# Optimization experiments

Measured on AMD Instinct MI355X. Metric: run time of the kernel, lower is better.

Reference implementation:

```python
import jax, jax.numpy as jnp
import numpy as np

N, D, K, V, H, F_ = 4096, 128, 64, 64, 4, 256
EPS = 1e-5


def _layer_norm(x, g, b):
    m = jnp.mean(x, axis=-1, keepdims=True)
    v = jnp.mean((x - m) ** 2, axis=-1, keepdims=True)
    return (x - m) * jax.lax.rsqrt(v + EPS) * g + b


def setup_inputs() -> dict:
    key = jax.random.key(0)
    ks = jax.random.split(key, 20)
    s_in = (2.0 / D) ** 0.5  # kaiming-ish scale for q/k/v projections
    inp = {
        "x": jax.random.normal(ks[0], (N, D), jnp.float32),
        "rpe": jax.random.normal(ks[1], (5, N, N), jnp.float32) * 0.02,
        "Wq": jax.random.normal(ks[2], (H, D, K), jnp.float32) * s_in,
        "bq": jnp.zeros((H, K), jnp.float32),
        "Wk": jax.random.normal(ks[3], (H, D, K), jnp.float32) * s_in,
        "bk": jnp.zeros((H, K), jnp.float32),
        "Wv": jax.random.normal(ks[4], (H, D, V), jnp.float32) * s_in,
        "bv": jnp.zeros((H, V), jnp.float32),
        "rpe_w": jax.random.normal(ks[5], (5,), jnp.float32) * (1.0 / 5.0) ** 0.5,
        "rpe_b": jnp.zeros((), jnp.float32),
        "Wo": jax.random.normal(ks[6], (H * V, D), jnp.float32) * (1.0 / (H * V)) ** 0.5,
        "bo": jnp.zeros((D,), jnp.float32),
        "W1": jax.random.normal(ks[7], (D, F_), jnp.float32) * (1.0 / D) ** 0.5,
        "b1": jnp.zeros((F_,), jnp.float32),
        "W2": jax.random.normal(ks[8], (F_, D), jnp.float32) * (1.0 / F_) ** 0.5,
        "b2": jnp.zeros((D,), jnp.float32),
        "ln1_g": jnp.ones((D,), jnp.float32),
        "ln1_b": jnp.zeros((D,), jnp.float32),
        "ln2_g": jnp.ones((D,), jnp.float32),
        "ln2_b": jnp.zeros((D,), jnp.float32),
    }
    return inp


def reference(x, rpe, Wq, bq, Wk, bk, Wv, bv, rpe_w, rpe_b, Wo, bo,
              W1, b1, W2, b2, ln1_g, ln1_b, ln2_g, ln2_b):
    # ReLU'd per-head projections (vectorized over heads): [H, N, K/V]
    q = jax.nn.relu(jnp.einsum("nd,hdk->hnk", x, Wq) + bq[:, None, :])
    k = jax.nn.relu(jnp.einsum("nd,hdk->hnk", x, Wk) + bk[:, None, :])
    v = jax.nn.relu(jnp.einsum("nd,hdv->hnv", x, Wv) + bv[:, None, :])
    scores = jnp.einsum("hnk,hmk->hnm", q, k) / jnp.sqrt(jnp.asarray(K, x.dtype))
    attn = jax.nn.softmax(scores, axis=-1)  # torch dim=1 on 2D == last axis
    o = jnp.einsum("hnm,hmv->hnv", attn, v)
    mho = jnp.transpose(o, (1, 0, 2)).reshape(N, H * V)  # concat heads
    # RPE: Linear(5->1) over channel axis -> [N, N], then left-matmul
    rpe_weights = jnp.einsum("fnm,f->nm", rpe, rpe_w) + rpe_b
    adjusted = rpe_weights @ mho
    proj = adjusted @ Wo + bo
    x1 = _layer_norm(x + proj, ln1_g, ln1_b)  # dropout is identity (eval)
    ffn = jax.nn.relu(x1 @ W1 + b1) @ W2 + b2
    return _layer_norm(x1 + ffn, ln2_g, ln2_b)
```

## Files before the change

kernel.cpp:

```cpp
#include <hip/hip_runtime.h>

typedef __attribute__((ext_vector_type(8))) short bf16x8;
typedef __attribute__((ext_vector_type(4))) float f32x4;

#define N_TOK 4096
#define NC_ATT 8
#define NC_GEMM 8

static __device__ __forceinline__ ushort f2bf(float f) {
    union { float f; unsigned u; } x; x.f = f;
    unsigned u = x.u;
    unsigned r = (u + 0x7FFFu + ((u >> 16) & 1u)) >> 16;
    return (ushort)r;
}
static __device__ __forceinline__ unsigned pkbf(float a, float b) {
    unsigned r;
    asm("v_cvt_pk_bf16_f32 %0, %1, %2" : "=v"(r) : "v"(a), "v"(b));
    return r;
}
static __device__ __forceinline__ float bf2f(ushort u) {
    union { unsigned u; float f; } x; x.u = (unsigned)u << 16; return x.f;
}

__global__ void prep_all(const float* __restrict__ x,
                         const float* __restrict__ Wq, const float* __restrict__ Wk,
                         const float* __restrict__ Wv, const float* __restrict__ Wo,
                         const float* __restrict__ W1, const float* __restrict__ W2,
                         ushort* __restrict__ xb, ushort* __restrict__ WqT,
                         ushort* __restrict__ WkT, ushort* __restrict__ WvT,
                         ushort* __restrict__ WoT, ushort* __restrict__ W1T,
                         ushort* __restrict__ W2T) {
    int i = blockIdx.x * 256 + threadIdx.x;
    if (i < 131072) {
        float4 v = ((const float4*)x)[i];
        ushort4 o;
        o.x = f2bf(v.x); o.y = f2bf(v.y); o.z = f2bf(v.z); o.w = f2bf(v.w);
        ((ushort4*)xb)[i] = o;
        return;
    }
    int j = i - 131072;
    int t = j >> 15, e = j & 32767;
    if (t < 3) {
        const float* src = (t == 0 ? Wq : t == 1 ? Wk : Wv);
        ushort* dst = (t == 0 ? WqT : t == 1 ? WkT : WvT);
        int h = e >> 13, rem = e & 8191, d = rem >> 6, k = rem & 63;
        dst[h * 8192 + k * 128 + d] = f2bf(src[e]);
    } else if (t == 3) {
        int r = e >> 7, c = e & 127;
        WoT[c * 256 + r] = f2bf(Wo[e]);
    } else if (t == 4) {
        int r = e >> 8, c = e & 255;
        W1T[c * 128 + r] = f2bf(W1[e]);
    } else {
        int r = e >> 7, c = e & 127;
        W2T[c * 256 + r] = f2bf(W2[e]);
    }
}

__global__ __launch_bounds__(256) void qkv_proj(
    const ushort* __restrict__ xb, const ushort* __restrict__ WqT,
    const ushort* __restrict__ WkT, const ushort* __restrict__ WvT,
    const float* __restrict__ bq, const float* __restrict__ bk, const float* __restrict__ bv,
    ushort* __restrict__ qb, ushort* __restrict__ kb, ushort* __restrict__ vT) {
    int m0 = blockIdx.x * 64;
    int h = blockIdx.y & 3, which = blockIdx.y >> 2;
    int wave = threadIdx.x >> 6, lane = threadIdx.x & 63;
    int fr = lane & 15, kg = lane >> 4;
    int wm = m0 + wave * 16;
    const ushort* WT = (which == 0 ? WqT : which == 1 ? WkT : WvT) + (long)h * 64 * 128;
    const float* bias = (which == 0 ? bq : which == 1 ? bk : bv) + h * 64;
    f32x4 acc[4] = {};
    for (int k0 = 0; k0 < 128; k0 += 32) {
        bf16x8 a = *(const bf16x8*)(xb + (long)(wm + fr) * 128 + k0 + kg * 8);
#pragma unroll
        for (int t = 0; t < 4; ++t) {
            bf16x8 b = *(const bf16x8*)(WT + (long)(t * 16 + fr) * 128 + k0 + kg * 8);
            acc[t] = __builtin_amdgcn_mfma_f32_16x16x32_bf16(a, b, acc[t], 0, 0, 0);
        }
    }
    int rb = wm + kg * 4;
#pragma unroll
    for (int t = 0; t < 4; ++t) {
        int col = t * 16 + fr;
        float bs = bias[col];
        if (which == 2) {
            ushort4 o;
            o.x = f2bf(fmaxf(acc[t][0] + bs, 0.f));
            o.y = f2bf(fmaxf(acc[t][1] + bs, 0.f));
            o.z = f2bf(fmaxf(acc[t][2] + bs, 0.f));
            o.w = f2bf(fmaxf(acc[t][3] + bs, 0.f));
            *(ushort4*)(vT + ((long)h * 64 + col) * N_TOK + rb) = o;
        } else {
            ushort* dst = (which == 0 ? qb : kb) + (long)h * N_TOK * 64;
            float scl = (which == 0) ? 0.125f * 1.44269504f : 1.0f;
#pragma unroll
            for (int r = 0; r < 4; ++r)
                dst[(long)(rb + r) * 64 + col] = f2bf(fmaxf(acc[t][r] + bs, 0.f) * scl);
        }
    }
}

__global__ __launch_bounds__(512, 6) void attn_flash2(
    const ushort* __restrict__ qb, const ushort* __restrict__ kb,
    const ushort* __restrict__ vT, ushort* __restrict__ opart,
    float* __restrict__ mlpart) {
    int qt = blockIdx.x, h = blockIdx.y, cz = blockIdx.z;
    int w = threadIdx.x >> 6, lane = threadIdx.x & 63;
    int fr = lane & 15, kg = lane >> 4;
    int lr = lane >> 3, lc = lane & 7;
    int swz = (lc ^ (lr & 7)) * 8;
    __shared__ ushort Kt[2][64 * 64];
    __shared__ ushort Vt[2][64 * 64];
    __shared__ ushort Pl[8][16 * 64];
    const ushort* qh = qb + (long)h * N_TOK * 64;
    const ushort* kh = kb + (long)h * N_TOK * 64;
    const ushort* vh = vT + (long)h * 64 * N_TOK;
    int q0 = qt * 128 + w * 16;
    bf16x8 qf0 = *(const bf16x8*)(qh + (long)(q0 + fr) * 64 + kg * 8);
    bf16x8 qf1 = *(const bf16x8*)(qh + (long)(q0 + fr) * 64 + 32 + kg * 8);
    f32x4 o[4] = {};
    float lsum = 0.f;
    int nbase = cz * (N_TOK / NC_ATT);
    auto stage = [&](int buf, int s) {
        int n0 = nbase + s * 64;
        int row = w * 8 + lr;
        __builtin_amdgcn_global_load_lds(
            (const __attribute__((address_space(1))) unsigned int*)(kh + (long)(n0 + row) * 64 + swz),
            (__attribute__((address_space(3))) unsigned int*)(&Kt[buf][w * 512]), 16, 0, 0);
        __builtin_amdgcn_global_load_lds(
            (const __attribute__((address_space(1))) unsigned int*)(vh + (long)row * N_TOK + n0 + swz),
            (__attribute__((address_space(3))) unsigned int*)(&Vt[buf][w * 512]), 16, 0, 0);
    };
    stage(0, 0);
    __syncthreads();
    const int NS = (N_TOK / NC_ATT) / 64;
    for (int s = 0; s < NS; ++s) {
        int buf = s & 1;
        if (s + 1 < NS) stage(buf ^ 1, s + 1);
        f32x4 sc[4] = {};
        __builtin_amdgcn_s_setprio(1);
#pragma unroll
        for (int t = 0; t < 4; ++t) {
            int row = t * 16 + fr;
            bf16x8 k0 = *(const bf16x8*)(&Kt[buf][row * 64 + ((kg * 8) ^ ((row & 7) * 8))]);
            bf16x8 k1 = *(const bf16x8*)(&Kt[buf][row * 64 + ((32 + kg * 8) ^ ((row & 7) * 8))]);
            sc[t] = __builtin_amdgcn_mfma_f32_16x16x32_bf16(k0, qf0, sc[t], 0, 0, 0);
            sc[t] = __builtin_amdgcn_mfma_f32_16x16x32_bf16(k1, qf1, sc[t], 0, 0, 0);
        }
        __builtin_amdgcn_s_setprio(0);
#pragma unroll
        for (int t = 0; t < 4; ++t)
#pragma unroll
            for (int r = 0; r < 4; ++r) {
                float p = exp2f(sc[t][r]);
                sc[t][r] = p;
                lsum += p;
            }
#pragma unroll
        for (int t = 0; t < 4; ++t) {
            uint2 u;
            u.x = pkbf(sc[t][0], sc[t][1]);
            u.y = pkbf(sc[t][2], sc[t][3]);
            *(uint2*)(&Pl[w][fr * 64 + ((t * 16 + kg * 4) ^ ((fr & 7) * 8))]) = u;
        }
        __builtin_amdgcn_s_setprio(1);
#pragma unroll
        for (int ks = 0; ks < 2; ++ks) {
            bf16x8 pf = *(const bf16x8*)(&Pl[w][fr * 64 + ((ks * 32 + kg * 8) ^ ((fr & 7) * 8))]);
#pragma unroll
            for (int t = 0; t < 4; ++t) {
                int row = t * 16 + fr;
                bf16x8 b = *(const bf16x8*)(&Vt[buf][row * 64 + ((ks * 32 + kg * 8) ^ ((row & 7) * 8))]);
                o[t] = __builtin_amdgcn_mfma_f32_16x16x32_bf16(pf, b, o[t], 0, 0, 0);
            }
        }
        __builtin_amdgcn_s_setprio(0);
        __syncthreads();
    }
    lsum += __shfl_xor(lsum, 16);
    lsum += __shfl_xor(lsum, 32);
    float linv = 1.0f / lsum;
    float lq[4];
#pragma unroll
    for (int r = 0; r < 4; ++r) lq[r] = __shfl(linv, kg * 4 + r);
    ushort* ob = opart + (((long)cz * 4 + h) * N_TOK + q0 + kg * 4) * 64;
#pragma unroll
    for (int t = 0; t < 4; ++t)
#pragma unroll
        for (int r = 0; r < 4; ++r)
            ob[(long)r * 64 + t * 16 + fr] = f2bf(o[t][r] * lq[r]);
    if (lane < 16)
        mlpart[((long)cz * 4 + h) * N_TOK + q0 + lane] = lsum;
}

__global__ __launch_bounds__(256) void combine_wo(
    const ushort* __restrict__ opart, const float* __restrict__ mlpart,
    const ushort* __restrict__ WoT, ushort* __restrict__ PT) {
    int q0 = blockIdx.x * 16;
    int tid = threadIdx.x;
    __shared__ ushort mt[16 * 256];
    {
        int q = tid >> 4, cg = tid & 15;
        int h = cg >> 2;
        long qg = q0 + q;
        float L = 0.f, co[NC_ATT];
#pragma unroll
        for (int c = 0; c < NC_ATT; ++c) {
            co[c] = mlpart[((long)c * 4 + h) * N_TOK + qg];
            L += co[c];
        }
        float inv = 1.0f / L;
#pragma unroll
        for (int c = 0; c < NC_ATT; ++c) co[c] *= inv;
        float a[16];
#pragma unroll
        for (int j = 0; j < 16; ++j) a[j] = 0.f;
#pragma unroll
        for (int c = 0; c < NC_ATT; ++c) {
            const ushort* pr = opart + (((long)c * 4 + h) * N_TOK + qg) * 64 + (cg & 3) * 16;
            bf16x8 v0 = *(const bf16x8*)(pr);
            bf16x8 v1 = *(const bf16x8*)(pr + 8);
#pragma unroll
            for (int j = 0; j < 8; ++j) {
                a[j] += co[c] * bf2f((ushort)v0[j]);
                a[8 + j] += co[c] * bf2f((ushort)v1[j]);
            }
        }
        int c0 = cg * 16;
#pragma unroll
        for (int g = 0; g < 4; ++g) {
            uint2 u;
            u.x = pkbf(a[g * 4 + 0], a[g * 4 + 1]);
            u.y = pkbf(a[g * 4 + 2], a[g * 4 + 3]);
            *(uint2*)(&mt[q * 256 + ((c0 + g * 4) ^ ((q & 7) * 8))]) = u;
        }
    }
    __syncthreads();
    {
        int w = tid >> 6, lane = tid & 63;
        int fr = lane & 15, kg = lane >> 4;
        f32x4 acc[2] = {};
        for (int k0 = 0; k0 < 256; k0 += 32) {
            bf16x8 a0 = *(const bf16x8*)(WoT + (long)(w * 32 + fr) * 256 + k0 + kg * 8);
            bf16x8 a1 = *(const bf16x8*)(WoT + (long)(w * 32 + 16 + fr) * 256 + k0 + kg * 8);
            bf16x8 b = *(const bf16x8*)(&mt[fr * 256 + ((k0 + kg * 8) ^ ((fr & 7) * 8))]);
            acc[0] = __builtin_amdgcn_mfma_f32_16x16x32_bf16(a0, b, acc[0], 0, 0, 0);
            acc[1] = __builtin_amdgcn_mfma_f32_16x16x32_bf16(a1, b, acc[1], 0, 0, 0);
        }
#pragma unroll
        for (int dt = 0; dt < 2; ++dt)
#pragma unroll
            for (int r = 0; r < 4; ++r)
                PT[(long)(w * 32 + dt * 16 + kg * 4 + r) * N_TOK + q0 + fr] =
                    f2bf(acc[dt][r]);
    }
}

__global__ __launch_bounds__(512) void gemm_big_fused(
    const float* __restrict__ rpe, const float* __restrict__ rpe_w,
    const float* __restrict__ rpe_b, const ushort* __restrict__ PT,
    float* __restrict__ part) {
    int mt = blockIdx.x, cz = blockIdx.y;
    int tid = threadIdx.x;
    int w = tid >> 6, lane = tid & 63;
    int fr = lane & 15, kg = lane >> 4;
    int lr = lane >> 3, lc = lane & 7;
    int swzB = (lc ^ (lr & 7)) * 8;
    int ms = w >> 1, nh = w & 1;
    __shared__ ushort At[64 * 256];
    __shared__ ushort Bt[2][128 * 64];
    int m0 = mt * 64;
    long kbase = (long)cz * (N_TOK / NC_GEMM);
    float w0 = rpe_w[0], w1 = rpe_w[1], w2 = rpe_w[2], w3 = rpe_w[3], w4 = rpe_w[4];
    float bb = rpe_b[0];
    const long PLANE = (long)N_TOK * N_TOK;
    int arow = ms * 16 + fr;
    int lrow = tid >> 3, seg = tid & 7;
    auto stage_B = [&](int buf, int sb) {
        const ushort* src = PT + kbase + sb * 64 + swzB;
#pragma unroll
        for (int j = 0; j < 2; ++j) {
            int i = w * 2 + j;
            int row = i * 8 + lr;
            __builtin_amdgcn_global_load_lds(
                (const __attribute__((address_space(1))) unsigned int*)(src + (long)row * N_TOK),
                (__attribute__((address_space(3))) unsigned int*)(&Bt[buf][i * 512]), 16, 0, 0);
        }
    };
    f32x4 acc[4] = {};
    for (int p = 0; p < 2; ++p) {
        if (p == 0) stage_B(0, 0);
        const float* base = rpe + (long)(m0 + lrow) * N_TOK + kbase + p * 256;
#pragma unroll
        for (int rnd = 0; rnd < 4; ++rnd) {
            float4 pv[2][5];
#pragma unroll
            for (int g = 0; g < 2; ++g) {
                int col = (seg + (rnd * 2 + g) * 8) * 4;
#pragma unroll
                for (int pl = 0; pl < 5; ++pl)
                    pv[g][pl] = *(const float4*)(base + col + pl * PLANE);
            }
#pragma unroll
            for (int g = 0; g < 2; ++g) {
                int col = (seg + (rnd * 2 + g) * 8) * 4;
                float4 a0 = pv[g][0], a1 = pv[g][1], a2 = pv[g][2], a3 = pv[g][3], a4 = pv[g][4];
                uint2 u;
                u.x = pkbf(bb + w0 * a0.x + w1 * a1.x + w2 * a2.x + w3 * a3.x + w4 * a4.x,
                           bb + w0 * a0.y + w1 * a1.y + w2 * a2.y + w3 * a3.y + w4 * a4.y);
                u.y = pkbf(bb + w0 * a0.z + w1 * a1.z + w2 * a2.z + w3 * a3.z + w4 * a4.z,
                           bb + w0 * a0.w + w1 * a1.w + w2 * a2.w + w3 * a3.w + w4 * a4.w);
                *(uint2*)(&At[lrow * 256 + (col ^ ((lrow & 7) * 8))]) = u;
            }
        }
        __syncthreads();
        for (int ks = 0; ks < 4; ++ks) {
            int sb = p * 4 + ks;
            if (sb + 1 < 8) stage_B((sb + 1) & 1, sb + 1);
#pragma unroll
            for (int k2 = 0; k2 < 2; ++k2) {
                int c = ks * 64 + k2 * 32 + kg * 8;
                bf16x8 av = *(const bf16x8*)(&At[arow * 256 + (c ^ ((arow & 7) * 8))]);
#pragma unroll
                for (int nf = 0; nf < 4; ++nf) {
                    int row = nh * 64 + nf * 16 + fr;
                    bf16x8 b = *(const bf16x8*)(&Bt[sb & 1][row * 64 + ((k2 * 32 + kg * 8) ^ ((row & 7) * 8))]);
                    acc[nf] = __builtin_amdgcn_mfma_f32_16x16x32_bf16(av, b, acc[nf], 0, 0, 0);
                }
            }
            __syncthreads();
        }
    }
    float* pb = part + ((long)cz * N_TOK + m0 + ms * 16 + kg * 4) * 128 + nh * 64 + fr;
#pragma unroll
    for (int nf = 0; nf < 4; ++nf)
#pragma unroll
        for (int r = 0; r < 4; ++r)
            pb[(long)r * 128 + nf * 16] = acc[nf][r];
}

__global__ __launch_bounds__(256) void megatail(
    const float* __restrict__ gpart, const float* __restrict__ bo,
    const float* __restrict__ x, const float* __restrict__ g1,
    const float* __restrict__ lb1, const ushort* __restrict__ W1T,
    const float* __restrict__ b1, const ushort* __restrict__ W2T,
    const float* __restrict__ b2, const float* __restrict__ g2,
    const float* __restrict__ lb2, float* __restrict__ out) {
    int r0 = blockIdx.x * 16;
    int tid = threadIdx.x;
    int w = tid >> 6, lane = tid & 63;
    int fr = lane & 15, kg = lane >> 4;
    __shared__ float x1f[16][132];
    __shared__ ushort x1b[16][128];
    __shared__ ushort hbuf[16][256];
    __shared__ float otile[16][132];
    int row = tid >> 4, c0 = (tid & 15) * 8;
    {
        float v[8];
        float4 s0 = {0.f, 0.f, 0.f, 0.f}, s1 = {0.f, 0.f, 0.f, 0.f};
#pragma unroll
        for (int c = 0; c < NC_GEMM; ++c) {
            const float* pr = gpart + ((long)c * N_TOK + r0 + row) * 128 + c0;
            float4 a = *(const float4*)(pr);
            float4 b = *(const float4*)(pr + 4);
            s0.x += a.x; s0.y += a.y; s0.z += a.z; s0.w += a.w;
            s1.x += b.x; s1.y += b.y; s1.z += b.z; s1.w += b.w;
        }
        const float* xr = x + (long)(r0 + row) * 128 + c0;
        v[0] = s0.x + bo[c0 + 0] + xr[0];
        v[1] = s0.y + bo[c0 + 1] + xr[1];
        v[2] = s0.z + bo[c0 + 2] + xr[2];
        v[3] = s0.w + bo[c0 + 3] + xr[3];
        v[4] = s1.x + bo[c0 + 4] + xr[4];
        v[5] = s1.y + bo[c0 + 5] + xr[5];
        v[6] = s1.z + bo[c0 + 6] + xr[6];
        v[7] = s1.w + bo[c0 + 7] + xr[7];
        float s = 0.f;
#pragma unroll
        for (int jj = 0; jj < 8; ++jj) s += v[jj];
#pragma unroll
        for (int off = 1; off < 16; off <<= 1) s += __shfl_xor(s, off);
        float mean = s * (1.0f / 128.0f);
        float ss = 0.f;
#pragma unroll
        for (int jj = 0; jj < 8; ++jj) { float d = v[jj] - mean; ss += d * d; }
#pragma unroll
        for (int off = 1; off < 16; off <<= 1) ss += __shfl_xor(ss, off);
        float rstd = rsqrtf(ss * (1.0f / 128.0f) + 1e-5f);
        union { bf16x8 vec; ushort us[8]; } pk8;
#pragma unroll
        for (int jj = 0; jj < 8; ++jj) {
            float y = (v[jj] - mean) * rstd * g1[c0 + jj] + lb1[c0 + jj];
            x1f[row][c0 + jj] = y;
            pk8.us[jj] = f2bf(y);
        }
        *(bf16x8*)(&x1b[row][c0 ^ ((row & 7) * 8)]) = pk8.vec;
    }
    __syncthreads();
    {
        f32x4 a1[4] = {};
#pragma unroll
        for (int ks = 0; ks < 4; ++ks) {
            bf16x8 a = *(const bf16x8*)(&x1b[fr][(ks * 32 + kg * 8) ^ ((fr & 7) * 8)]);
#pragma unroll
            for (int t = 0; t < 4; ++t) {
                bf16x8 b = *(const bf16x8*)(W1T + (long)(w * 64 + t * 16 + fr) * 128 + ks * 32 + kg * 8);
                a1[t] = __builtin_amdgcn_mfma_f32_16x16x32_bf16(a, b, a1[t], 0, 0, 0);
            }
        }
#pragma unroll
        for (int t = 0; t < 4; ++t) {
            int col = w * 64 + t * 16 + fr;
            float bs = b1[col];
#pragma unroll
            for (int r = 0; r < 4; ++r) {
                int rr = kg * 4 + r;
                hbuf[rr][col ^ ((rr & 7) * 8)] = f2bf(fmaxf(a1[t][r] + bs, 0.f));
            }
        }
    }
    __syncthreads();
    {
        f32x4 a2[2] = {};
#pragma unroll
        for (int ks = 0; ks < 8; ++ks) {
            bf16x8 a = *(const bf16x8*)(&hbuf[fr][(ks * 32 + kg * 8) ^ ((fr & 7) * 8)]);
#pragma unroll
            for (int t = 0; t < 2; ++t) {
                bf16x8 b = *(const bf16x8*)(W2T + (long)(w * 32 + t * 16 + fr) * 256 + ks * 32 + kg * 8);
                a2[t] = __builtin_amdgcn_mfma_f32_16x16x32_bf16(a, b, a2[t], 0, 0, 0);
            }
        }
#pragma unroll
        for (int t = 0; t < 2; ++t) {
            int col = w * 32 + t * 16 + fr;
            float bs = b2[col];
#pragma unroll
            for (int r = 0; r < 4; ++r) {
                int rr = kg * 4 + r;
                otile[rr][col] = a2[t][r] + bs + x1f[rr][col];
            }
        }
    }
    __syncthreads();
    {
        float v[8];
        float s = 0.f;
#pragma unroll
        for (int jj = 0; jj < 8; ++jj) { v[jj] = otile[row][c0 + jj]; s += v[jj]; }
#pragma unroll
        for (int off = 1; off < 16; off <<= 1) s += __shfl_xor(s, off);
        float mean = s * (1.0f / 128.0f);
        float ss = 0.f;
#pragma unroll
        for (int jj = 0; jj < 8; ++jj) { float d = v[jj] - mean; ss += d * d; }
#pragma unroll
        for (int off = 1; off < 16; off <<= 1) ss += __shfl_xor(ss, off);
        float rstd = rsqrtf(ss * (1.0f / 128.0f) + 1e-5f);
#pragma unroll
        for (int jj = 0; jj < 8; ++jj) {
            float y = (v[jj] - mean) * rstd * g2[c0 + jj] + lb2[c0 + jj];
            out[(long)(r0 + row) * 128 + c0 + jj] = y;
        }
    }
}

extern "C" void kernel_launch(void* const* d_in, const int* in_sizes, int n_in,
                              void* d_out, int out_size, void* d_ws, size_t ws_size,
                              hipStream_t stream) {
    const float* x     = (const float*)d_in[0];
    const float* rpe   = (const float*)d_in[1];
    const float* Wq    = (const float*)d_in[2];
    const float* bq    = (const float*)d_in[3];
    const float* Wk    = (const float*)d_in[4];
    const float* bk    = (const float*)d_in[5];
    const float* Wv    = (const float*)d_in[6];
    const float* bv    = (const float*)d_in[7];
    const float* rpe_w = (const float*)d_in[8];
    const float* rpe_b = (const float*)d_in[9];
    const float* Wo    = (const float*)d_in[10];
    const float* bo    = (const float*)d_in[11];
    const float* W1    = (const float*)d_in[12];
    const float* b1    = (const float*)d_in[13];
    const float* W2    = (const float*)d_in[14];
    const float* b2    = (const float*)d_in[15];
    const float* g1    = (const float*)d_in[16];
    const float* lb1   = (const float*)d_in[17];
    const float* g2    = (const float*)d_in[18];
    const float* lb2   = (const float*)d_in[19];

    char* wp = (char*)d_ws;
    auto alloc = [&](size_t sz) { char* p = wp; wp += (sz + 255) & ~(size_t)255; return p; };
    ushort* xb    = (ushort*)alloc((size_t)4096 * 128 * 2);
    ushort* WqT   = (ushort*)alloc((size_t)4 * 64 * 128 * 2);
    ushort* WkT   = (ushort*)alloc((size_t)4 * 64 * 128 * 2);
    ushort* WvT   = (ushort*)alloc((size_t)4 * 64 * 128 * 2);
    ushort* WoT   = (ushort*)alloc((size_t)128 * 256 * 2);
    ushort* W1T   = (ushort*)alloc((size_t)256 * 128 * 2);
    ushort* W2T   = (ushort*)alloc((size_t)128 * 256 * 2);
    ushort* qb    = (ushort*)alloc((size_t)4 * 4096 * 64 * 2);
    ushort* kbuf  = (ushort*)alloc((size_t)4 * 4096 * 64 * 2);
    ushort* vT    = (ushort*)alloc((size_t)4 * 64 * 4096 * 2);
    ushort* PTb   = (ushort*)alloc((size_t)128 * 4096 * 2);
    ushort* opart = (ushort*)alloc((size_t)NC_ATT * 4 * 4096 * 64 * 2);
    float*  mlprt = (float*)alloc((size_t)NC_ATT * 4 * 4096 * 4);
    float*  gpart = (float*)alloc((size_t)NC_GEMM * 4096 * 128 * 4);

    prep_all<<<1280, 256, 0, stream>>>(x, Wq, Wk, Wv, Wo, W1, W2,
                                       xb, WqT, WkT, WvT, WoT, W1T, W2T);
    qkv_proj<<<dim3(64, 12), 256, 0, stream>>>(xb, WqT, WkT, WvT, bq, bk, bv, qb, kbuf, vT);
    attn_flash2<<<dim3(32, 4, NC_ATT), 512, 0, stream>>>(qb, kbuf, vT, opart, mlprt);
    combine_wo<<<256, 256, 0, stream>>>(opart, mlprt, WoT, PTb);
    gemm_big_fused<<<dim3(64, NC_GEMM), 512, 0, stream>>>(rpe, rpe_w, rpe_b, PTb, gpart);
    megatail<<<256, 256, 0, stream>>>(gpart, bo, x, g1, lb1, W1T, b1, W2T, b2,
                                      g2, lb2, (float*)d_out);
}
```

Measured before the change: 140.9 us.

## Overlap RPE channel reduction with attention via interleaved blocks in one launch

The 5-plane RPE reduction to bf16 moves out of the big GEMM and into the attention launch. Even-numbered blocks stream rpe and write a bf16 rpeW matrix, while odd-numbered blocks run flash attention, so the memory-bound reduction overlaps the compute-bound attention. The big GEMM then becomes a plain bf16 GEMM that double-buffers both operands with async global-to-LDS loads and raises wave priority around the MFMA section. This costs an extra 32MB bf16 write and re-read of rpeW, and the mixed block types may compete for CU resources.

Result: faster. 135.3 us (-4.0%).

```diff
diff --git a/kernel.cpp b/kernel.cpp
--- a/kernel.cpp
+++ b/kernel.cpp
@@ -100,18 +100,44 @@
     }
 }
 
-__global__ __launch_bounds__(512, 6) void attn_flash2(
+__global__ __launch_bounds__(512, 6) void fused_rpe_attn(
+    const float* __restrict__ rpe, const float* __restrict__ rpe_w,
+    const float* __restrict__ rpe_b, ushort* __restrict__ rpeW,
     const ushort* __restrict__ qb, const ushort* __restrict__ kb,
     const ushort* __restrict__ vT, ushort* __restrict__ opart,
     float* __restrict__ mlpart) {
-    int qt = blockIdx.x, h = blockIdx.y, cz = blockIdx.z;
+    __shared__ ushort Kt[2][64 * 64];
+    __shared__ ushort Vt[2][64 * 64];
+    __shared__ ushort Pl[8][16 * 64];
+    int bid = blockIdx.x;
+    int idx = bid >> 1;
+    if ((bid & 1) == 0) {
+        const long QUADS = (long)N_TOK * N_TOK / 4;
+        float w0 = rpe_w[0], w1 = rpe_w[1], w2 = rpe_w[2], w3 = rpe_w[3], w4 = rpe_w[4];
+        float bb = rpe_b[0];
+        const float4* p = (const float4*)rpe;
+        for (long i = (long)idx * 512 + threadIdx.x; i < QUADS; i += (long)1024 * 512) {
+            float4 a0 = p[i];
+            float4 a1 = p[i + QUADS];
+            float4 a2 = p[i + 2 * QUADS];
+            float4 a3 = p[i + 3 * QUADS];
+            float4 a4 = p[i + 4 * QUADS];
+            ushort4 o;
+            unsigned lo = pkbf(bb + w0 * a0.x + w1 * a1.x + w2 * a2.x + w3 * a3.x + w4 * a4.x,
+                               bb + w0 * a0.y + w1 * a1.y + w2 * a2.y + w3 * a3.y + w4 * a4.y);
+            unsigned hi = pkbf(bb + w0 * a0.z + w1 * a1.z + w2 * a2.z + w3 * a3.z + w4 * a4.z,
+                               bb + w0 * a0.w + w1 * a1.w + w2 * a2.w + w3 * a3.w + w4 * a4.w);
+            o.x = (ushort)lo; o.y = (ushort)(lo >> 16);
+            o.z = (ushort)hi; o.w = (ushort)(hi >> 16);
+            ((ushort4*)rpeW)[i] = o;
+        }
+        return;
+    }
+    int qt = idx & 31, h = (idx >> 5) & 3, cz = idx >> 7;
     int w = threadIdx.x >> 6, lane = threadIdx.x & 63;
     int fr = lane & 15, kg = lane >> 4;
     int lr = lane >> 3, lc = lane & 7;
     int swz = (lc ^ (lr & 7)) * 8;
-    __shared__ ushort Kt[2][64 * 64];
-    __shared__ ushort Vt[2][64 * 64];
-    __shared__ ushort Pl[8][16 * 64];
     const ushort* qh = qb + (long)h * N_TOK * 64;
     const ushort* kh = kb + (long)h * N_TOK * 64;
     const ushort* vh = vT + (long)h * 64 * N_TOK;
@@ -256,80 +282,56 @@
     }
 }
 
-__global__ __launch_bounds__(512) void gemm_big_fused(
-    const float* __restrict__ rpe, const float* __restrict__ rpe_w,
-    const float* __restrict__ rpe_b, const ushort* __restrict__ PT,
+__global__ __launch_bounds__(512) void gemm_big2(
+    const ushort* __restrict__ A, const ushort* __restrict__ PT,
     float* __restrict__ part) {
     int mt = blockIdx.x, cz = blockIdx.y;
     int tid = threadIdx.x;
     int w = tid >> 6, lane = tid & 63;
     int fr = lane & 15, kg = lane >> 4;
     int lr = lane >> 3, lc = lane & 7;
-    int swzB = (lc ^ (lr & 7)) * 8;
+    int swz = (lc ^ (lr & 7)) * 8;
     int ms = w >> 1, nh = w & 1;
-    __shared__ ushort At[64 * 256];
+    __shared__ ushort At[2][64 * 64];
     __shared__ ushort Bt[2][128 * 64];
     int m0 = mt * 64;
     long kbase = (long)cz * (N_TOK / NC_GEMM);
-    float w0 = rpe_w[0], w1 = rpe_w[1], w2 = rpe_w[2], w3 = rpe_w[3], w4 = rpe_w[4];
-    float bb = rpe_b[0];
-    const long PLANE = (long)N_TOK * N_TOK;
     int arow = ms * 16 + fr;
-    int lrow = tid >> 3, seg = tid & 7;
-    auto stage_B = [&](int buf, int sb) {
-        const ushort* src = PT + kbase + sb * 64 + swzB;
+    auto stage = [&](int buf, int s) {
+        long kc = kbase + s * 64 + swz;
+        int rowA = w * 8 + lr;
+        __builtin_amdgcn_global_load_lds(
+            (const __attribute__((address_space(1))) unsigned int*)(A + (long)(m0 + rowA) * N_TOK + kc),
+            (__attribute__((address_space(3))) unsigned int*)(&At[buf][w * 512]), 16, 0, 0);
 #pragma unroll
         for (int j = 0; j < 2; ++j) {
-            int i = w * 2 + j;
-            int row = i * 8 + lr;
+            int row = w * 16 + j * 8 + lr;
             __builtin_amdgcn_global_load_lds(
-                (const __attribute__((address_space(1))) unsigned int*)(src + (long)row * N_TOK),
-                (__attribute__((address_space(3))) unsigned int*)(&Bt[buf][i * 512]), 16, 0, 0);
+                (const __attribute__((address_space(1))) unsigned int*)(PT + (long)row * N_TOK + kc),
+                (__attribute__((address_space(3))) unsigned int*)(&Bt[buf][(w * 2 + j) * 512]), 16, 0, 0);
         }
     };
     f32x4 acc[4] = {};
-    for (int p = 0; p < 2; ++p) {
-        if (p == 0) stage_B(0, 0);
-        const float* base = rpe + (long)(m0 + lrow) * N_TOK + kbase + p * 256;
-#pragma unroll
-        for (int rnd = 0; rnd < 4; ++rnd) {
-            float4 pv[2][5];
-#pragma unroll
-            for (int g = 0; g < 2; ++g) {
-                int col = (seg + (rnd * 2 + g) * 8) * 4;
-#pragma unroll
-                for (int pl = 0; pl < 5; ++pl)
-                    pv[g][pl] = *(const float4*)(base + col + pl * PLANE);
-            }
-#pragma unroll
-            for (int g = 0; g < 2; ++g) {
-                int col = (seg + (rnd * 2 + g) * 8) * 4;
-                float4 a0 = pv[g][0], a1 = pv[g][1], a2 = pv[g][2], a3 = pv[g][3], a4 = pv[g][4];
-                uint2 u;
-                u.x = pkbf(bb + w0 * a0.x + w1 * a1.x + w2 * a2.x + w3 * a3.x + w4 * a4.x,
-                           bb + w0 * a0.y + w1 * a1.y + w2 * a2.y + w3 * a3.y + w4 * a4.y);
-                u.y = pkbf(bb + w0 * a0.z + w1 * a1.z + w2 * a2.z + w3 * a3.z + w4 * a4.z,
-                           bb + w0 * a0.w + w1 * a1.w + w2 * a2.w + w3 * a3.w + w4 * a4.w);
-                *(uint2*)(&At[lrow * 256 + (col ^ ((lrow & 7) * 8))]) = u;
-            }
-        }
+    stage(0, 0);
+    __syncthreads();
+    const int NS = (N_TOK / NC_GEMM) / 64;
+    for (int s = 0; s < NS; ++s) {
+        int buf = s & 1;
+        if (s + 1 < NS) stage(buf ^ 1, s + 1);
+        __builtin_amdgcn_s_setprio(1);
+#pragma unroll
+        for (int ks = 0; ks < 2; ++ks) {
+            int c = ks * 32 + kg * 8;
+            bf16x8 av = *(const bf16x8*)(&At[buf][arow * 64 + (c ^ ((arow & 7) * 8))]);
+#pragma unroll
+            for (int nf = 0; nf < 4; ++nf) {
+                int row = nh * 64 + nf * 16 + fr;
+                bf16x8 b = *(const bf16x8*)(&Bt[buf][row * 64 + (c ^ ((row & 7) * 8))]);
+                acc[nf] = __builtin_amdgcn_mfma_f32_16x16x32_bf16(av, b, acc[nf], 0, 0, 0);
+            }
+        }
+        __builtin_amdgcn_s_setprio(0);
         __syncthreads();
-        for (int ks = 0; ks < 4; ++ks) {
-            int sb = p * 4 + ks;
-            if (sb + 1 < 8) stage_B((sb + 1) & 1, sb + 1);
-#pragma unroll
-            for (int k2 = 0; k2 < 2; ++k2) {
-                int c = ks * 64 + k2 * 32 + kg * 8;
-                bf16x8 av = *(const bf16x8*)(&At[arow * 256 + (c ^ ((arow & 7) * 8))]);
-#pragma unroll
-                for (int nf = 0; nf < 4; ++nf) {
-                    int row = nh * 64 + nf * 16 + fr;
-                    bf16x8 b = *(const bf16x8*)(&Bt[sb & 1][row * 64 + ((k2 * 32 + kg * 8) ^ ((row & 7) * 8))]);
-                    acc[nf] = __builtin_amdgcn_mfma_f32_16x16x32_bf16(av, b, acc[nf], 0, 0, 0);
-                }
-            }
-            __syncthreads();
-        }
     }
     float* pb = part + ((long)cz * N_TOK + m0 + ms * 16 + kg * 4) * 128 + nh * 64 + fr;
 #pragma unroll
@@ -501,6 +503,7 @@
     ushort* qb    = (ushort*)alloc((size_t)4 * 4096 * 64 * 2);
     ushort* kbuf  = (ushort*)alloc((size_t)4 * 4096 * 64 * 2);
     ushort* vT    = (ushort*)alloc((size_t)4 * 64 * 4096 * 2);
+    ushort* rpeW  = (ushort*)alloc((size_t)4096 * 4096 * 2);
     ushort* PTb   = (ushort*)alloc((size_t)128 * 4096 * 2);
     ushort* opart = (ushort*)alloc((size_t)NC_ATT * 4 * 4096 * 64 * 2);
     float*  mlprt = (float*)alloc((size_t)NC_ATT * 4 * 4096 * 4);
@@ -509,9 +512,10 @@
     prep_all<<<1280, 256, 0, stream>>>(x, Wq, Wk, Wv, Wo, W1, W2,
                                        xb, WqT, WkT, WvT, WoT, W1T, W2T);
     qkv_proj<<<dim3(64, 12), 256, 0, stream>>>(xb, WqT, WkT, WvT, bq, bk, bv, qb, kbuf, vT);
-    attn_flash2<<<dim3(32, 4, NC_ATT), 512, 0, stream>>>(qb, kbuf, vT, opart, mlprt);
+    fused_rpe_attn<<<2048, 512, 0, stream>>>(rpe, rpe_w, rpe_b, rpeW,
+                                             qb, kbuf, vT, opart, mlprt);
     combine_wo<<<256, 256, 0, stream>>>(opart, mlprt, WoT, PTb);
-    gemm_big_fused<<<dim3(64, NC_GEMM), 512, 0, stream>>>(rpe, rpe_w, rpe_b, PTb, gpart);
+    gemm_big2<<<dim3(64, NC_GEMM), 512, 0, stream>>>(rpeW, PTb, gpart);
     megatail<<<256, 256, 0, stream>>>(gpart, bo, x, g1, lb1, W1T, b1, W2T, b2,
                                       g2, lb2, (float*)d_out);
 }
```
